# Kernel tuning notes

Hardware: AMD Instinct MI355X
Metric: run time of the kernel (lower is better)

Reference implementation:

```python
import jax, jax.numpy as jnp
import numpy as np
from jax import lax

B, T = 256, 64
X_DIMS, CCG_DIMS, H, N_TAG = 512, 256, 1024, 512
DIN = X_DIMS + CCG_DIMS
PAD = 0


def setup_inputs() -> dict:
    key = jax.random.key(0)
    ks = jax.random.split(key, 12)
    emb = jax.random.normal(ks[0], (N_TAG, CCG_DIMS), jnp.float32)
    emb = emb.at[PAD].set(0.0)  # padding_idx row is zero
    s_ih = 1.0 / np.sqrt(H)
    return {
        "x": jax.random.normal(ks[1], (B, X_DIMS), jnp.float32),
        "atom_truth": jax.random.randint(ks[2], (B, T), 0, N_TAG),
        "atom_mask": jax.random.randint(ks[3], (B, T), 0, 2).astype(bool),
        "emb": emb,
        "W_ih": jax.random.normal(ks[4], (4 * H, DIN), jnp.float32) * s_ih,
        "W_hh": jax.random.normal(ks[5], (4 * H, H), jnp.float32) * s_ih,
        "b_ih": jax.random.normal(ks[6], (4 * H,), jnp.float32) * s_ih,
        "b_hh": jax.random.normal(ks[7], (4 * H,), jnp.float32) * s_ih,
        "W_out": jax.random.normal(ks[8], (N_TAG, H), jnp.float32) * s_ih,
        "b_out": jax.random.normal(ks[9], (N_TAG,), jnp.float32) * s_ih,
        "h0": jax.random.normal(ks[10], (B, H), jnp.float32),
        "c0": jax.random.normal(ks[11], (B, H), jnp.float32),
    }


def reference(x, atom_truth, atom_mask, emb, W_ih, W_hh, b_ih, b_hh, W_out, b_out, h0, c0):
    b, t = atom_truth.shape
    # teacher forcing: step 0 uses token 0, step k uses atom_truth[:, k-1]
    prev_tok = jnp.concatenate([jnp.zeros((b, 1), atom_truth.dtype), atom_truth[:, :-1]], axis=1)
    ccg = emb[prev_tok]                                      # [B,T,E]
    inp = jnp.concatenate([jnp.broadcast_to(x[:, None, :], (b, t, x.shape[1])), ccg], axis=-1)
    # precompute input projection for all steps: [B,T,4H]
    xproj = jnp.einsum('btd,gd->btg', inp, W_ih) + b_ih + b_hh

    def cell(carry, xt):                                     # xt: [B,4H]
        h, c = carry
        gates = xt + h @ W_hh.T
        i, f, g, o = jnp.split(gates, 4, axis=-1)            # torch gate order i,f,g,o
        i, f, o = jax.nn.sigmoid(i), jax.nn.sigmoid(f), jax.nn.sigmoid(o)
        g = jnp.tanh(g)
        c = f * c + i * g
        h = o * jnp.tanh(c)
        return (h, c), h

    _, hs = lax.scan(cell, (h0, c0), jnp.swapaxes(xproj, 0, 1))  # hs: [T,B,H]
    logits = hs @ W_out.T + b_out                            # [T,B,N_TAG]
    logp = jax.nn.log_softmax(logits, axis=-1)
    tgt = atom_truth.T                                       # [T,B]
    nll = -jnp.take_along_axis(logp, tgt[..., None], axis=-1)[..., 0]  # [T,B]
    mask = atom_mask.T.astype(nll.dtype)
    return jnp.sum(nll * mask) / jnp.sum(mask)


if __name__ == "__main__":
    print(reference(**setup_inputs()))
```

## Files before the change

### kernel.cpp

```cpp
#include <hip/hip_runtime.h>
#include <hip/hip_bf16.h>

#define BB 256
#define TT 64
#define XD 512
#define CCG 256
#define DINk 768
#define HH 1024
#define G4 4096
#define NTAG 512

typedef float f32x4 __attribute__((ext_vector_type(4)));
typedef short s16x8 __attribute__((ext_vector_type(8)));
typedef short s16x4 __attribute__((ext_vector_type(4)));

#define WS_HS    0ull
#define WS_XBASE (WS_HS + (size_t)(TT+1)*BB*HH*2)
#define WS_EPROJ (WS_XBASE + (size_t)BB*G4*4)
#define WS_WIH   (WS_EPROJ + (size_t)NTAG*G4*4)
#define WS_WOUT  (WS_WIH + (size_t)G4*DINk*2)
#define WS_XBF   (WS_WOUT + (size_t)NTAG*HH*2)
#define WS_EMBBF (WS_XBF + (size_t)BB*XD*2)
#define WS_CNT   (WS_EMBBF + (size_t)NTAG*CCG*2)
#define WS_ACC   (WS_CNT + 1024)
#define WS_FLAG  (WS_ACC + 64)
#define WS_XPROJ (WS_FLAG + 64)

static __device__ __forceinline__ short f2bf(float f) {
  __hip_bfloat16 h = __float2bfloat16(f);
  return __builtin_bit_cast(short, h);
}
static __device__ __forceinline__ float bf2f(unsigned short u) {
  unsigned x = ((unsigned)u) << 16;
  return __builtin_bit_cast(float, x);
}
static __device__ __forceinline__ void store_dword_cc(void* p, unsigned v) {
  asm volatile("global_store_dword %0, %1, off sc0 sc1" :: "v"(p), "v"(v) : "memory");
}
static __device__ __forceinline__ void store_short_cc(void* p, unsigned v) {
  asm volatile("global_store_short %0, %1, off sc0 sc1" :: "v"(p), "v"(v) : "memory");
}
static __device__ __forceinline__ int load_int_cc(const void* p) {
  int r;
  asm volatile("global_load_dword %0, %1, off sc0 sc1\n\ts_waitcnt vmcnt(0)"
               : "=v"(r) : "v"(p) : "memory");
  return r;
}
static __device__ __forceinline__ float fsig(float x) {
  return __builtin_amdgcn_rcpf(1.f + __expf(-x));
}
static __device__ __forceinline__ float ftanh(float x) {
  return 1.f - 2.f * __builtin_amdgcn_rcpf(1.f + __expf(2.f * x));
}

__global__ void k_f2bf8(const float* __restrict__ in, short* __restrict__ out, int n8) {
  int i = blockIdx.x * blockDim.x + threadIdx.x;
  if (i >= n8) return;
  size_t idx = (size_t)i * 8;
  float4 a = *(const float4*)(in + idx);
  float4 b = *(const float4*)(in + idx + 4);
  s16x8 o;
  o[0]=f2bf(a.x); o[1]=f2bf(a.y); o[2]=f2bf(a.z); o[3]=f2bf(a.w);
  o[4]=f2bf(b.x); o[5]=f2bf(b.y); o[6]=f2bf(b.z); o[7]=f2bf(b.w);
  *(s16x8*)(out + idx) = o;
}

__global__ void k_init(const float* __restrict__ h0, const int* __restrict__ mask_as_int,
                       char* __restrict__ ws) {
  int tid = blockIdx.x * blockDim.x + threadIdx.x;
  short* hb0 = (short*)(ws + WS_HS);
  for (int i = tid; i < BB * HH; i += gridDim.x * blockDim.x) hb0[i] = f2bf(h0[i]);
  if (blockIdx.x == 0) {
    int* cnt = (int*)(ws + WS_CNT);
    for (int i = threadIdx.x; i < 256; i += blockDim.x) cnt[i] = 0;
    int v = 0;
    for (int i = threadIdx.x; i < 4096; i += blockDim.x) v |= (mask_as_int[i] & ~1);
    __shared__ int red[256];
    red[threadIdx.x] = v;
    __syncthreads();
    if (threadIdx.x == 0) {
      int a = 0;
      for (int j = 0; j < 256; j++) a |= red[j];
      ((int*)(ws + WS_FLAG))[0] = (a != 0) ? 1 : 0;
      float* acc = (float*)(ws + WS_ACC);
      acc[0] = 0.f; acc[1] = 0.f;
    }
  }
}

__global__ __launch_bounds__(256) void k_gemm(const short* __restrict__ A, int lda,
    const short* __restrict__ Bm, int ldb, int bcol0,
    short* __restrict__ C, int ldc, int ksteps,
    const float* __restrict__ bias1, const float* __restrict__ bias2) {
  int w = threadIdx.x >> 6, l = threadIdx.x & 63;
  int lc = l & 15, lq = l >> 4;
  int arow = blockIdx.x * 64 + w * 16 + lc;
  f32x4 acc[4];
  const f32x4 z = {0.f, 0.f, 0.f, 0.f};
#pragma unroll
  for (int i = 0; i < 4; i++) acc[i] = z;
  const short* ap = A + (size_t)arow * lda + lq * 8;
  for (int kk = 0; kk < ksteps; ++kk) {
    s16x8 a = *(const s16x8*)(ap + kk * 32);
#pragma unroll
    for (int nt = 0; nt < 4; ++nt) {
      int brow = blockIdx.y * 64 + nt * 16 + lc;
      s16x8 b = *(const s16x8*)(Bm + (size_t)brow * ldb + bcol0 + kk * 32 + lq * 8);
      acc[nt] = __builtin_amdgcn_mfma_f32_16x16x32_bf16(a, b, acc[nt], 0, 0, 0);
    }
  }
#pragma unroll
  for (int nt = 0; nt < 4; ++nt) {
    int col = blockIdx.y * 64 + nt * 16 + lc;
    float badd = (bias1 ? bias1[col] : 0.f) + (bias2 ? bias2[col] : 0.f);
#pragma unroll
    for (int j = 0; j < 4; j++) {
      int r = blockIdx.x * 64 + w * 16 + lq * 4 + j;
      C[(size_t)r * ldc + col] = f2bf(acc[nt][j] + badd);
    }
  }
}

__global__ __launch_bounds__(256) void k_xproj_t(const short* __restrict__ xb,
    const short* __restrict__ ep, const int* __restrict__ atruth,
    short* __restrict__ out) {
  __shared__ short tile[64 * 264];
  const int cc = blockIdx.x, g = blockIdx.y, t = blockIdx.z;
  const int b = threadIdx.x;
  const int tok = (t == 0) ? 0 : atruth[b * TT + t - 1];
  const int gc0 = g * 1024 + cc * 64;
  const short* xs = xb + (size_t)b * G4 + gc0;
  const short* es = ep + (size_t)tok * G4 + gc0;
#pragma unroll
  for (int i = 0; i < 64; i += 8) {
    s16x8 xv = *(const s16x8*)(xs + i);
    s16x8 ev = *(const s16x8*)(es + i);
#pragma unroll
    for (int j = 0; j < 8; ++j)
      tile[(i + j) * 264 + b] = f2bf(bf2f((unsigned short)xv[j]) + bf2f((unsigned short)ev[j]));
  }
  __syncthreads();
  const int c = threadIdx.x >> 2, b0 = (threadIdx.x & 3) * 64;
  short* dst = out + ((size_t)t * G4 + gc0 + c) * BB + b0;
  const short* src = tile + c * 264 + b0;
#pragma unroll
  for (int i = 0; i < 64; i += 8) *(s16x8*)(dst + i) = *(const s16x8*)(src + i);
}

__global__ __launch_bounds__(512, 2) void k_lstm(const float* __restrict__ Whh,
    const short* __restrict__ xproj, const float* __restrict__ c0,
    char* __restrict__ ws) {
  extern __shared__ char sm[];
  float* part = (float*)(sm + 131072);
  const int bid = blockIdx.x;
  const int xcd = bid & 7, slot = bid >> 3;
  const int mg = xcd >> 1;
  const int hb = slot * 2 + (xcd & 1);
  const int wgid = (xcd & 1) * 32 + slot;
  const int tid = threadIdx.x;
  const int w = tid >> 6, l = tid & 63;
  const int lc = l & 15, lq = l >> 4;
  const int wy = w & 3, kh = w >> 2;

  {
    const int r = tid >> 3, q = tid & 7;
    const int g = r >> 4, rl = r & 15;
    const float* src = Whh + (size_t)(g * HH + hb * 16 + rl) * HH + q * 128;
    const int swz = (rl & 7) << 4;
    char* dst = sm + r * 2048;
#pragma unroll
    for (int i = 0; i < 128; i += 8) {
      float4 f0 = *(const float4*)(src + i);
      float4 f1 = *(const float4*)(src + i + 4);
      s16x8 o;
      o[0]=f2bf(f0.x); o[1]=f2bf(f0.y); o[2]=f2bf(f0.z); o[3]=f2bf(f0.w);
      o[4]=f2bf(f1.x); o[5]=f2bf(f1.y); o[6]=f2bf(f1.z); o[7]=f2bf(f1.w);
      int koff = (q * 128 + i) * 2;
      *(s16x8*)(dst + (koff ^ swz)) = o;
    }
  }

  const int colbase = hb * 16;
  short* hs = (short*)(ws + WS_HS);
  int* flags = (int*)(ws + WS_CNT);
  const int swzl = (lc & 7) << 4;
  const int row0 = mg * 64 + wy * 16;

  float cst[4];
  if (kh == 0) {
#pragma unroll
    for (int j = 0; j < 4; ++j)
      cst[j] = c0[(size_t)(row0 + lq * 4 + j) * HH + colbase + lc];
  }
  float* pslot = part + ((size_t)wy * 64 + l) * 20;
  __syncthreads();

  for (int t = 0; t < TT; ++t) {
    s16x4 xg0, xg1, xg2, xg3;
    if (kh == 0) {
      const short* xp = xproj + ((size_t)t * G4 + colbase + lc) * BB + row0 + lq * 4;
      xg0 = *(const s16x4*)(xp);
      xg1 = *(const s16x4*)(xp + (size_t)1024 * BB);
      xg2 = *(const s16x4*)(xp + (size_t)2048 * BB);
      xg3 = *(const s16x4*)(xp + (size_t)3072 * BB);
    }

    if (t && w == 0) {
      const int* f = flags + mg * 64 + l;
      for (;;) {
        int v = load_int_cc(f);
        if (__all(v >= t)) break;
        __builtin_amdgcn_s_sleep(4);
      }
    }
    __syncthreads();

    const f32x4 z = {0.f, 0.f, 0.f, 0.f};
    f32x4 acc0 = z, acc1 = z, acc2 = z, acc3 = z;
    const short* arowp = hs + (size_t)t * (BB * HH) + (size_t)(row0 + lc) * HH + kh * 512 + lq * 8;
#pragma unroll
    for (int kk = 0; kk < 16; ++kk) {
      s16x8 a = *(const s16x8*)(arowp + kk * 32);
      const int kx = (((kh * 16 + kk) * 64) + lq * 16) ^ swzl;
      const char* bp = sm + lc * 2048 + kx;
      acc0 = __builtin_amdgcn_mfma_f32_16x16x32_bf16(a, *(const s16x8*)(bp), acc0, 0, 0, 0);
      acc1 = __builtin_amdgcn_mfma_f32_16x16x32_bf16(a, *(const s16x8*)(bp + 16 * 2048), acc1, 0, 0, 0);
      acc2 = __builtin_amdgcn_mfma_f32_16x16x32_bf16(a, *(const s16x8*)(bp + 32 * 2048), acc2, 0, 0, 0);
      acc3 = __builtin_amdgcn_mfma_f32_16x16x32_bf16(a, *(const s16x8*)(bp + 48 * 2048), acc3, 0, 0, 0);
    }

    if (kh == 1) {
      *(f32x4*)(pslot) = acc0;
      *(f32x4*)(pslot + 4) = acc1;
      *(f32x4*)(pslot + 8) = acc2;
      *(f32x4*)(pslot + 12) = acc3;
    }
    __syncthreads();

    if (kh == 0) {
      acc0 += *(const f32x4*)(pslot);
      acc1 += *(const f32x4*)(pslot + 4);
      acc2 += *(const f32x4*)(pslot + 8);
      acc3 += *(const f32x4*)(pslot + 12);
      short* hrow = hs + (size_t)(t + 1) * (BB * HH) + (size_t)(row0 + lq * 4) * HH + colbase + lc;
#pragma unroll
      for (int j = 0; j < 4; ++j) {
        float pi = acc0[j] + bf2f((unsigned short)xg0[j]);
        float pf = acc1[j] + bf2f((unsigned short)xg1[j]);
        float pg = acc2[j] + bf2f((unsigned short)xg2[j]);
        float po = acc3[j] + bf2f((unsigned short)xg3[j]);
        float cv = fsig(pf) * cst[j] + fsig(pi) * ftanh(pg);
        cst[j] = cv;
        float hv = fsig(po) * ftanh(cv);
        store_short_cc(hrow + (size_t)j * HH, (unsigned)(unsigned short)f2bf(hv));
      }
    }
    asm volatile("s_waitcnt vmcnt(0)" ::: "memory");
    __syncthreads();
    if (tid == 0 && t < TT - 1) store_dword_cc(flags + mg * 64 + wgid, t + 1);
  }
}

__global__ __launch_bounds__(256, 1) void k_logits(const short* __restrict__ hsb,
    const short* __restrict__ Wo, const float* __restrict__ bout,
    const int* __restrict__ atruth, const void* __restrict__ maskp,
    char* __restrict__ ws) {
  extern __shared__ char sm[];
  const int tid = threadIdx.x;
  const int w = tid >> 6, l = tid & 63;
  const int lc = l & 15, lq = l >> 4;
  const int rowbase = blockIdx.x * 64 + w * 16;
  f32x4 acc[32];
#pragma unroll
  for (int nt = 0; nt < 32; ++nt) {
    float bv = bout[nt * 16 + lc];
    f32x4 tmp = {bv, bv, bv, bv};
    acc[nt] = tmp;
  }
  const int swzl = (lc & 7) << 4;
  for (int kb = 0; kb < 16; ++kb) {
    __syncthreads();
    {
      const int r0 = tid >> 3, q = tid & 7;
#pragma unroll
      for (int i = 0; i < 16; i++) {
        int r = r0 + 32 * i;
        s16x8 v = *(const s16x8*)(Wo + (size_t)r * HH + kb * 64 + q * 8);
        *(s16x8*)(sm + r * 128 + ((q * 16) ^ ((r & 7) << 4))) = v;
      }
    }
    __syncthreads();
#pragma unroll
    for (int ks = 0; ks < 2; ++ks) {
      s16x8 a = *(const s16x8*)(hsb + (size_t)(rowbase + lc) * HH + kb * 64 + ks * 32 + lq * 8);
      const int kx = (ks * 64 + lq * 16) ^ swzl;
#pragma unroll
      for (int nt = 0; nt < 32; ++nt) {
        s16x8 b = *(const s16x8*)(sm + (nt * 16 + lc) * 128 + kx);
        acc[nt] = __builtin_amdgcn_mfma_f32_16x16x32_bf16(a, b, acc[nt], 0, 0, 0);
      }
    }
  }
  const int bytemode = ((const int*)(ws + WS_FLAG))[0];
  const unsigned char* mb = (const unsigned char*)maskp;
  const int* mi = (const int*)maskp;
  float nlls = 0.f, cnts = 0.f;
#pragma unroll
  for (int j = 0; j < 4; j++) {
    int gr = rowbase + lq * 4 + j;
    int tt = gr >> 8, b = gr & 255;
    float m = -1e30f;
#pragma unroll
    for (int nt = 0; nt < 32; ++nt) m = fmaxf(m, acc[nt][j]);
    m = fmaxf(m, __shfl_xor(m, 1)); m = fmaxf(m, __shfl_xor(m, 2));
    m = fmaxf(m, __shfl_xor(m, 4)); m = fmaxf(m, __shfl_xor(m, 8));
    float s = 0.f;
#pragma unroll
    for (int nt = 0; nt < 32; ++nt) s += __expf(acc[nt][j] - m);
    s += __shfl_xor(s, 1); s += __shfl_xor(s, 2);
    s += __shfl_xor(s, 4); s += __shfl_xor(s, 8);
    float lse = m + __logf(s);
    int tg = atruth[b * TT + tt];
    int mk = bytemode ? (int)mb[b * TT + tt] : mi[b * TT + tt];
    if (((tg & 15) == lc) && mk) {
      float tl = 0.f;
#pragma unroll
      for (int nt = 0; nt < 32; ++nt) if (nt == (tg >> 4)) tl = acc[nt][j];
      nlls += (lse - tl);
    }
    if (lc == 0 && mk) cnts += 1.f;
  }
#pragma unroll
  for (int off = 1; off < 64; off <<= 1) {
    nlls += __shfl_xor(nlls, off);
    cnts += __shfl_xor(cnts, off);
  }
  if (l == 0) {
    float* accf = (float*)(ws + WS_ACC);
    atomicAdd(&accf[0], nlls);
    atomicAdd(&accf[1], cnts);
  }
}

__global__ void k_final(const char* __restrict__ ws, float* __restrict__ out) {
  const float* accf = (const float*)(ws + WS_ACC);
  out[0] = accf[0] / accf[1];
}

extern "C" void kernel_launch(void* const* d_in, const int* in_sizes, int n_in,
                              void* d_out, int out_size, void* d_ws, size_t ws_size,
                              hipStream_t stream) {
  const float* x      = (const float*)d_in[0];
  const int*   atruth = (const int*)d_in[1];
  const void*  amask  = d_in[2];
  const float* emb    = (const float*)d_in[3];
  const float* W_ih   = (const float*)d_in[4];
  const float* W_hh   = (const float*)d_in[5];
  const float* b_ih   = (const float*)d_in[6];
  const float* b_hh   = (const float*)d_in[7];
  const float* W_out  = (const float*)d_in[8];
  const float* b_out  = (const float*)d_in[9];
  const float* h0     = (const float*)d_in[10];
  const float* c0     = (const float*)d_in[11];
  char* ws = (char*)d_ws;
  float* out = (float*)d_out;

  hipFuncSetAttribute((const void*)k_lstm, hipFuncAttributeMaxDynamicSharedMemorySize, 151552);
  hipFuncSetAttribute((const void*)k_logits, hipFuncAttributeMaxDynamicSharedMemorySize, 65536);

  k_f2bf8<<<dim3((G4 * DINk / 8 + 255) / 256), 256, 0, stream>>>(W_ih, (short*)(ws + WS_WIH), G4 * DINk / 8);
  k_f2bf8<<<dim3((NTAG * HH / 8 + 255) / 256), 256, 0, stream>>>(W_out, (short*)(ws + WS_WOUT), NTAG * HH / 8);
  k_f2bf8<<<dim3((BB * XD / 8 + 255) / 256), 256, 0, stream>>>(x, (short*)(ws + WS_XBF), BB * XD / 8);
  k_f2bf8<<<dim3((NTAG * CCG / 8 + 255) / 256), 256, 0, stream>>>(emb, (short*)(ws + WS_EMBBF), NTAG * CCG / 8);

  k_init<<<64, 256, 0, stream>>>(h0, (const int*)amask, ws);

  k_gemm<<<dim3(4, 64), 256, 0, stream>>>((short*)(ws + WS_XBF), XD, (short*)(ws + WS_WIH), DINk, 0,
                                          (short*)(ws + WS_XBASE), G4, XD / 32, b_ih, b_hh);
  k_gemm<<<dim3(8, 64), 256, 0, stream>>>((short*)(ws + WS_EMBBF), CCG, (short*)(ws + WS_WIH), DINk, XD,
                                          (short*)(ws + WS_EPROJ), G4, CCG / 32, nullptr, nullptr);

  k_xproj_t<<<dim3(16, 4, 64), 256, 0, stream>>>((const short*)(ws + WS_XBASE),
                                                 (const short*)(ws + WS_EPROJ), atruth,
                                                 (short*)(ws + WS_XPROJ));

  k_lstm<<<256, 512, 151552, stream>>>(W_hh, (const short*)(ws + WS_XPROJ), c0, ws);

  k_logits<<<256, 256, 65536, stream>>>((short*)(ws + WS_HS) + BB * HH, (short*)(ws + WS_WOUT), b_out,
                                        atruth, amask, ws);
  k_final<<<1, 1, 0, stream>>>(ws, out);
}
```

Before: 589.8 us.

## Keep W_hh slice in registers and split K four ways in LSTM kernel

```diff
diff --git a/kernel.cpp b/kernel.cpp
--- a/kernel.cpp
+++ b/kernel.cpp
@@ -151,7 +151,7 @@
     const short* __restrict__ xproj, const float* __restrict__ c0,
     char* __restrict__ ws) {
   extern __shared__ char sm[];
-  float* part = (float*)(sm + 131072);
+  float* part = (float*)sm;
   const int bid = blockIdx.x;
   const int xcd = bid & 7, slot = bid >> 3;
   const int mg = xcd >> 1;
@@ -160,49 +160,46 @@
   const int tid = threadIdx.x;
   const int w = tid >> 6, l = tid & 63;
   const int lc = l & 15, lq = l >> 4;
-  const int wy = w & 3, kh = w >> 2;
-
-  {
-    const int r = tid >> 3, q = tid & 7;
-    const int g = r >> 4, rl = r & 15;
-    const float* src = Whh + (size_t)(g * HH + hb * 16 + rl) * HH + q * 128;
-    const int swz = (rl & 7) << 4;
-    char* dst = sm + r * 2048;
-#pragma unroll
-    for (int i = 0; i < 128; i += 8) {
-      float4 f0 = *(const float4*)(src + i);
-      float4 f1 = *(const float4*)(src + i + 4);
+  const int wy = w & 1, kq = w >> 1;
+
+  const int colbase = hb * 16;
+  short* hs = (short*)(ws + WS_HS);
+  int* flags = (int*)(ws + WS_CNT);
+  const int arow0 = mg * 64 + wy * 32;
+
+  s16x8 breg[4][8];
+#pragma unroll
+  for (int g = 0; g < 4; ++g) {
+    const float* wr = Whh + (size_t)(g * HH + colbase + lc) * HH + kq * 256 + lq * 8;
+#pragma unroll
+    for (int s = 0; s < 8; ++s) {
+      float4 f0 = *(const float4*)(wr + s * 32);
+      float4 f1 = *(const float4*)(wr + s * 32 + 4);
       s16x8 o;
       o[0]=f2bf(f0.x); o[1]=f2bf(f0.y); o[2]=f2bf(f0.z); o[3]=f2bf(f0.w);
       o[4]=f2bf(f1.x); o[5]=f2bf(f1.y); o[6]=f2bf(f1.z); o[7]=f2bf(f1.w);
-      int koff = (q * 128 + i) * 2;
-      *(s16x8*)(dst + (koff ^ swz)) = o;
-    }
-  }
-
-  const int colbase = hb * 16;
-  short* hs = (short*)(ws + WS_HS);
-  int* flags = (int*)(ws + WS_CNT);
-  const int swzl = (lc & 7) << 4;
-  const int row0 = mg * 64 + wy * 16;
-
-  float cst[4];
-  if (kh == 0) {
-#pragma unroll
-    for (int j = 0; j < 4; ++j)
-      cst[j] = c0[(size_t)(row0 + lq * 4 + j) * HH + colbase + lc];
-  }
-  float* pslot = part + ((size_t)wy * 64 + l) * 20;
-  __syncthreads();
+      breg[g][s] = o;
+    }
+  }
+
+  float cst[2][4];
+  if (kq == 0) {
+#pragma unroll
+    for (int rt = 0; rt < 2; ++rt)
+#pragma unroll
+      for (int j = 0; j < 4; ++j)
+        cst[rt][j] = c0[(size_t)(arow0 + rt * 16 + lq * 4 + j) * HH + colbase + lc];
+  }
 
   for (int t = 0; t < TT; ++t) {
-    s16x4 xg0, xg1, xg2, xg3;
-    if (kh == 0) {
-      const short* xp = xproj + ((size_t)t * G4 + colbase + lc) * BB + row0 + lq * 4;
-      xg0 = *(const s16x4*)(xp);
-      xg1 = *(const s16x4*)(xp + (size_t)1024 * BB);
-      xg2 = *(const s16x4*)(xp + (size_t)2048 * BB);
-      xg3 = *(const s16x4*)(xp + (size_t)3072 * BB);
+    s16x4 xg[2][4];
+    if (kq == 0) {
+#pragma unroll
+      for (int rt = 0; rt < 2; ++rt)
+#pragma unroll
+        for (int g = 0; g < 4; ++g)
+          xg[rt][g] = *(const s16x4*)(xproj +
+              ((size_t)t * G4 + g * HH + colbase + lc) * BB + arow0 + rt * 16 + lq * 4);
     }
 
     if (t && w == 0) {
@@ -210,49 +207,63 @@
       for (;;) {
         int v = load_int_cc(f);
         if (__all(v >= t)) break;
-        __builtin_amdgcn_s_sleep(4);
+        __builtin_amdgcn_s_sleep(1);
       }
     }
     __syncthreads();
 
     const f32x4 z = {0.f, 0.f, 0.f, 0.f};
-    f32x4 acc0 = z, acc1 = z, acc2 = z, acc3 = z;
-    const short* arowp = hs + (size_t)t * (BB * HH) + (size_t)(row0 + lc) * HH + kh * 512 + lq * 8;
-#pragma unroll
-    for (int kk = 0; kk < 16; ++kk) {
-      s16x8 a = *(const s16x8*)(arowp + kk * 32);
-      const int kx = (((kh * 16 + kk) * 64) + lq * 16) ^ swzl;
-      const char* bp = sm + lc * 2048 + kx;
-      acc0 = __builtin_amdgcn_mfma_f32_16x16x32_bf16(a, *(const s16x8*)(bp), acc0, 0, 0, 0);
-      acc1 = __builtin_amdgcn_mfma_f32_16x16x32_bf16(a, *(const s16x8*)(bp + 16 * 2048), acc1, 0, 0, 0);
-      acc2 = __builtin_amdgcn_mfma_f32_16x16x32_bf16(a, *(const s16x8*)(bp + 32 * 2048), acc2, 0, 0, 0);
-      acc3 = __builtin_amdgcn_mfma_f32_16x16x32_bf16(a, *(const s16x8*)(bp + 48 * 2048), acc3, 0, 0, 0);
-    }
-
-    if (kh == 1) {
-      *(f32x4*)(pslot) = acc0;
-      *(f32x4*)(pslot + 4) = acc1;
-      *(f32x4*)(pslot + 8) = acc2;
-      *(f32x4*)(pslot + 12) = acc3;
-    }
-    __syncthreads();
-
-    if (kh == 0) {
-      acc0 += *(const f32x4*)(pslot);
-      acc1 += *(const f32x4*)(pslot + 4);
-      acc2 += *(const f32x4*)(pslot + 8);
-      acc3 += *(const f32x4*)(pslot + 12);
-      short* hrow = hs + (size_t)(t + 1) * (BB * HH) + (size_t)(row0 + lq * 4) * HH + colbase + lc;
-#pragma unroll
-      for (int j = 0; j < 4; ++j) {
-        float pi = acc0[j] + bf2f((unsigned short)xg0[j]);
-        float pf = acc1[j] + bf2f((unsigned short)xg1[j]);
-        float pg = acc2[j] + bf2f((unsigned short)xg2[j]);
-        float po = acc3[j] + bf2f((unsigned short)xg3[j]);
-        float cv = fsig(pf) * cst[j] + fsig(pi) * ftanh(pg);
-        cst[j] = cv;
-        float hv = fsig(po) * ftanh(cv);
-        store_short_cc(hrow + (size_t)j * HH, (unsigned)(unsigned short)f2bf(hv));
+    f32x4 acc[2][4];
+#pragma unroll
+    for (int rt = 0; rt < 2; ++rt)
+#pragma unroll
+      for (int g = 0; g < 4; ++g) acc[rt][g] = z;
+    const short* ab = hs + (size_t)t * (BB * HH) + (size_t)(arow0 + lc) * HH + kq * 256 + lq * 8;
+#pragma unroll
+    for (int s = 0; s < 8; ++s) {
+      s16x8 a0 = *(const s16x8*)(ab + s * 32);
+      s16x8 a1 = *(const s16x8*)(ab + 16 * HH + s * 32);
+#pragma unroll
+      for (int g = 0; g < 4; ++g) {
+        acc[0][g] = __builtin_amdgcn_mfma_f32_16x16x32_bf16(a0, breg[g][s], acc[0][g], 0, 0, 0);
+        acc[1][g] = __builtin_amdgcn_mfma_f32_16x16x32_bf16(a1, breg[g][s], acc[1][g], 0, 0, 0);
+      }
+    }
+
+    if (kq) {
+      float* ps = part + (size_t)(((kq - 1) * 2 + wy) * 64 + l) * 36;
+#pragma unroll
+      for (int rt = 0; rt < 2; ++rt)
+#pragma unroll
+        for (int g = 0; g < 4; ++g)
+          *(f32x4*)(ps + (rt * 4 + g) * 4) = acc[rt][g];
+    }
+    __syncthreads();
+
+    if (kq == 0) {
+#pragma unroll
+      for (int q = 0; q < 3; ++q) {
+        const float* ps = part + (size_t)((q * 2 + wy) * 64 + l) * 36;
+#pragma unroll
+        for (int rt = 0; rt < 2; ++rt)
+#pragma unroll
+          for (int g = 0; g < 4; ++g)
+            acc[rt][g] += *(const f32x4*)(ps + (rt * 4 + g) * 4);
+      }
+#pragma unroll
+      for (int rt = 0; rt < 2; ++rt) {
+        short* hrow = hs + (size_t)(t + 1) * (BB * HH) +
+                      (size_t)(arow0 + rt * 16 + lq * 4) * HH + colbase + lc;
+#pragma unroll
+        for (int j = 0; j < 4; ++j) {
+          float pi = acc[rt][0][j] + bf2f((unsigned short)xg[rt][0][j]);
+          float pf = acc[rt][1][j] + bf2f((unsigned short)xg[rt][1][j]);
+          float pg = acc[rt][2][j] + bf2f((unsigned short)xg[rt][2][j]);
+          float po = acc[rt][3][j] + bf2f((unsigned short)xg[rt][3][j]);
+          float cv = fsig(pf) * cst[rt][j] + fsig(pi) * ftanh(pg);
+          cst[rt][j] = cv;
+          store_short_cc(hrow + (size_t)j * HH, (unsigned)(unsigned short)f2bf(fsig(po) * ftanh(cv)));
+        }
       }
     }
     asm volatile("s_waitcnt vmcnt(0)" ::: "memory");
@@ -365,7 +376,7 @@
   char* ws = (char*)d_ws;
   float* out = (float*)d_out;
 
-  hipFuncSetAttribute((const void*)k_lstm, hipFuncAttributeMaxDynamicSharedMemorySize, 151552);
+  hipFuncSetAttribute((const void*)k_lstm, hipFuncAttributeMaxDynamicSharedMemorySize, 55296);
   hipFuncSetAttribute((const void*)k_logits, hipFuncAttributeMaxDynamicSharedMemorySize, 65536);
 
   k_f2bf8<<<dim3((G4 * DINk / 8 + 255) / 256), 256, 0, stream>>>(W_ih, (short*)(ws + WS_WIH), G4 * DINk / 8);
@@ -384,7 +395,7 @@
                                                  (const short*)(ws + WS_EPROJ), atruth,
                                                  (short*)(ws + WS_XPROJ));
 
-  k_lstm<<<256, 512, 151552, stream>>>(W_hh, (const short*)(ws + WS_XPROJ), c0, ws);
+  k_lstm<<<256, 512, 55296, stream>>>(W_hh, (const short*)(ws + WS_XPROJ), c0, ws);
 
   k_logits<<<256, 256, 65536, stream>>>((short*)(ws + WS_HS) + BB * HH, (short*)(ws + WS_WOUT), b_out,
                                         atruth, amask, ws);
```

Result: slower. 628.7 us (+6.6%).

## Use per-wave step flags and vectorized flag polling in recurrent LSTM kernel

Applied to the files above, without the earlier changes.

```diff
diff --git a/kernel.cpp b/kernel.cpp
--- a/kernel.cpp
+++ b/kernel.cpp
@@ -22,7 +22,7 @@
 #define WS_XBF   (WS_WOUT + (size_t)NTAG*HH*2)
 #define WS_EMBBF (WS_XBF + (size_t)BB*XD*2)
 #define WS_CNT   (WS_EMBBF + (size_t)NTAG*CCG*2)
-#define WS_ACC   (WS_CNT + 1024)
+#define WS_ACC   (WS_CNT + 4096)
 #define WS_FLAG  (WS_ACC + 64)
 #define WS_XPROJ (WS_FLAG + 64)
 
@@ -40,9 +40,9 @@
 static __device__ __forceinline__ void store_short_cc(void* p, unsigned v) {
   asm volatile("global_store_short %0, %1, off sc0 sc1" :: "v"(p), "v"(v) : "memory");
 }
-static __device__ __forceinline__ int load_int_cc(const void* p) {
-  int r;
-  asm volatile("global_load_dword %0, %1, off sc0 sc1\n\ts_waitcnt vmcnt(0)"
+static __device__ __forceinline__ int4 load_int4_cc(const void* p) {
+  int4 r;
+  asm volatile("global_load_dwordx4 %0, %1, off sc0 sc1\n\ts_waitcnt vmcnt(0)"
                : "=v"(r) : "v"(p) : "memory");
   return r;
 }
@@ -72,7 +72,7 @@
   for (int i = tid; i < BB * HH; i += gridDim.x * blockDim.x) hb0[i] = f2bf(h0[i]);
   if (blockIdx.x == 0) {
     int* cnt = (int*)(ws + WS_CNT);
-    for (int i = threadIdx.x; i < 256; i += blockDim.x) cnt[i] = 0;
+    for (int i = threadIdx.x; i < 1024; i += blockDim.x) cnt[i] = 0;
     int v = 0;
     for (int i = threadIdx.x; i < 4096; i += blockDim.x) v |= (mask_as_int[i] & ~1);
     __shared__ int red[256];
@@ -182,7 +182,7 @@
 
   const int colbase = hb * 16;
   short* hs = (short*)(ws + WS_HS);
-  int* flags = (int*)(ws + WS_CNT);
+  int* flags4 = (int*)(ws + WS_CNT);
   const int swzl = (lc & 7) << 4;
   const int row0 = mg * 64 + wy * 16;
 
@@ -196,21 +196,20 @@
   __syncthreads();
 
   for (int t = 0; t < TT; ++t) {
-    s16x4 xg0, xg1, xg2, xg3;
+    s16x4 xg[4];
     if (kh == 0) {
-      const short* xp = xproj + ((size_t)t * G4 + colbase + lc) * BB + row0 + lq * 4;
-      xg0 = *(const s16x4*)(xp);
-      xg1 = *(const s16x4*)(xp + (size_t)1024 * BB);
-      xg2 = *(const s16x4*)(xp + (size_t)2048 * BB);
-      xg3 = *(const s16x4*)(xp + (size_t)3072 * BB);
+#pragma unroll
+      for (int g = 0; g < 4; ++g)
+        xg[g] = *(const s16x4*)(xproj +
+            ((size_t)t * G4 + g * HH + colbase + lc) * BB + row0 + lq * 4);
     }
 
     if (t && w == 0) {
-      const int* f = flags + mg * 64 + l;
+      const int4* f = (const int4*)flags4 + (mg * 64 + l);
       for (;;) {
-        int v = load_int_cc(f);
-        if (__all(v >= t)) break;
-        __builtin_amdgcn_s_sleep(4);
+        int4 v = load_int4_cc(f);
+        if (__all((v.x >= t) && (v.y >= t) && (v.z >= t) && (v.w >= t))) break;
+        __builtin_amdgcn_s_sleep(1);
       }
     }
     __syncthreads();
@@ -242,22 +241,22 @@
       acc1 += *(const f32x4*)(pslot + 4);
       acc2 += *(const f32x4*)(pslot + 8);
       acc3 += *(const f32x4*)(pslot + 12);
-      short* hrow = hs + (size_t)(t + 1) * (BB * HH) + (size_t)(row0 + lq * 4) * HH + colbase + lc;
+      short* hrow = hs + (size_t)(t + 1) * (BB * HH) +
+                    (size_t)(row0 + lq * 4) * HH + colbase + lc;
 #pragma unroll
       for (int j = 0; j < 4; ++j) {
-        float pi = acc0[j] + bf2f((unsigned short)xg0[j]);
-        float pf = acc1[j] + bf2f((unsigned short)xg1[j]);
-        float pg = acc2[j] + bf2f((unsigned short)xg2[j]);
-        float po = acc3[j] + bf2f((unsigned short)xg3[j]);
+        float pi = acc0[j] + bf2f((unsigned short)xg[0][j]);
+        float pf = acc1[j] + bf2f((unsigned short)xg[1][j]);
+        float pg = acc2[j] + bf2f((unsigned short)xg[2][j]);
+        float po = acc3[j] + bf2f((unsigned short)xg[3][j]);
         float cv = fsig(pf) * cst[j] + fsig(pi) * ftanh(pg);
         cst[j] = cv;
-        float hv = fsig(po) * ftanh(cv);
-        store_short_cc(hrow + (size_t)j * HH, (unsigned)(unsigned short)f2bf(hv));
+        store_short_cc(hrow + (size_t)j * HH, (unsigned)(unsigned short)f2bf(fsig(po) * ftanh(cv)));
       }
-    }
-    asm volatile("s_waitcnt vmcnt(0)" ::: "memory");
-    __syncthreads();
-    if (tid == 0 && t < TT - 1) store_dword_cc(flags + mg * 64 + wgid, t + 1);
+      asm volatile("s_waitcnt vmcnt(0)" ::: "memory");
+      if (l == 0 && t < TT - 1)
+        store_dword_cc(flags4 + (mg * 64 + wgid) * 4 + wy, t + 1);
+    }
   }
 }
 
```

After: 625.4 us. 1.06x slower.

## Prefetch next-step xproj, batch h loads, and relayout LSTM partial sums

Applied to the files above, without the earlier changes.

```diff
diff --git a/kernel.cpp b/kernel.cpp
--- a/kernel.cpp
+++ b/kernel.cpp
@@ -187,62 +187,77 @@
   const int row0 = mg * 64 + wy * 16;
 
   float cst[4];
+  s16x4 xg0, xg1, xg2, xg3, xn0, xn1, xn2, xn3;
   if (kh == 0) {
 #pragma unroll
     for (int j = 0; j < 4; ++j)
       cst[j] = c0[(size_t)(row0 + lq * 4 + j) * HH + colbase + lc];
-  }
-  float* pslot = part + ((size_t)wy * 64 + l) * 20;
+    const short* xp = xproj + ((size_t)colbase + lc) * BB + row0 + lq * 4;
+    xg0 = *(const s16x4*)(xp);
+    xg1 = *(const s16x4*)(xp + (size_t)1024 * BB);
+    xg2 = *(const s16x4*)(xp + (size_t)2048 * BB);
+    xg3 = *(const s16x4*)(xp + (size_t)3072 * BB);
+  }
+  float* pslot = part + (size_t)wy * 1024 + l;
   __syncthreads();
 
   for (int t = 0; t < TT; ++t) {
-    s16x4 xg0, xg1, xg2, xg3;
-    if (kh == 0) {
-      const short* xp = xproj + ((size_t)t * G4 + colbase + lc) * BB + row0 + lq * 4;
-      xg0 = *(const s16x4*)(xp);
-      xg1 = *(const s16x4*)(xp + (size_t)1024 * BB);
-      xg2 = *(const s16x4*)(xp + (size_t)2048 * BB);
-      xg3 = *(const s16x4*)(xp + (size_t)3072 * BB);
-    }
-
     if (t && w == 0) {
       const int* f = flags + mg * 64 + l;
       for (;;) {
         int v = load_int_cc(f);
         if (__all(v >= t)) break;
-        __builtin_amdgcn_s_sleep(4);
-      }
-    }
-    __syncthreads();
+        __builtin_amdgcn_s_sleep(1);
+      }
+    }
+    __syncthreads();
+
+    if (kh == 0 && t + 1 < TT) {
+      const short* xp = xproj + ((size_t)(t + 1) * G4 + colbase + lc) * BB + row0 + lq * 4;
+      xn0 = *(const s16x4*)(xp);
+      xn1 = *(const s16x4*)(xp + (size_t)1024 * BB);
+      xn2 = *(const s16x4*)(xp + (size_t)2048 * BB);
+      xn3 = *(const s16x4*)(xp + (size_t)3072 * BB);
+    }
+
+    const short* arowp = hs + (size_t)t * (BB * HH) + (size_t)(row0 + lc) * HH + kh * 512 + lq * 8;
+    s16x8 areg[16];
+#pragma unroll
+    for (int kk = 0; kk < 16; ++kk) areg[kk] = *(const s16x8*)(arowp + kk * 32);
 
     const f32x4 z = {0.f, 0.f, 0.f, 0.f};
     f32x4 acc0 = z, acc1 = z, acc2 = z, acc3 = z;
-    const short* arowp = hs + (size_t)t * (BB * HH) + (size_t)(row0 + lc) * HH + kh * 512 + lq * 8;
 #pragma unroll
     for (int kk = 0; kk < 16; ++kk) {
-      s16x8 a = *(const s16x8*)(arowp + kk * 32);
       const int kx = (((kh * 16 + kk) * 64) + lq * 16) ^ swzl;
       const char* bp = sm + lc * 2048 + kx;
-      acc0 = __builtin_amdgcn_mfma_f32_16x16x32_bf16(a, *(const s16x8*)(bp), acc0, 0, 0, 0);
-      acc1 = __builtin_amdgcn_mfma_f32_16x16x32_bf16(a, *(const s16x8*)(bp + 16 * 2048), acc1, 0, 0, 0);
-      acc2 = __builtin_amdgcn_mfma_f32_16x16x32_bf16(a, *(const s16x8*)(bp + 32 * 2048), acc2, 0, 0, 0);
-      acc3 = __builtin_amdgcn_mfma_f32_16x16x32_bf16(a, *(const s16x8*)(bp + 48 * 2048), acc3, 0, 0, 0);
+      acc0 = __builtin_amdgcn_mfma_f32_16x16x32_bf16(areg[kk], *(const s16x8*)(bp), acc0, 0, 0, 0);
+      acc1 = __builtin_amdgcn_mfma_f32_16x16x32_bf16(areg[kk], *(const s16x8*)(bp + 16 * 2048), acc1, 0, 0, 0);
+      acc2 = __builtin_amdgcn_mfma_f32_16x16x32_bf16(areg[kk], *(const s16x8*)(bp + 32 * 2048), acc2, 0, 0, 0);
+      acc3 = __builtin_amdgcn_mfma_f32_16x16x32_bf16(areg[kk], *(const s16x8*)(bp + 48 * 2048), acc3, 0, 0, 0);
     }
 
     if (kh == 1) {
-      *(f32x4*)(pslot) = acc0;
-      *(f32x4*)(pslot + 4) = acc1;
-      *(f32x4*)(pslot + 8) = acc2;
-      *(f32x4*)(pslot + 12) = acc3;
+#pragma unroll
+      for (int j = 0; j < 4; ++j) {
+        pslot[(0 * 4 + j) * 64] = acc0[j];
+        pslot[(1 * 4 + j) * 64] = acc1[j];
+        pslot[(2 * 4 + j) * 64] = acc2[j];
+        pslot[(3 * 4 + j) * 64] = acc3[j];
+      }
     }
     __syncthreads();
 
     if (kh == 0) {
-      acc0 += *(const f32x4*)(pslot);
-      acc1 += *(const f32x4*)(pslot + 4);
-      acc2 += *(const f32x4*)(pslot + 8);
-      acc3 += *(const f32x4*)(pslot + 12);
-      short* hrow = hs + (size_t)(t + 1) * (BB * HH) + (size_t)(row0 + lq * 4) * HH + colbase + lc;
+#pragma unroll
+      for (int j = 0; j < 4; ++j) {
+        acc0[j] += pslot[(0 * 4 + j) * 64];
+        acc1[j] += pslot[(1 * 4 + j) * 64];
+        acc2[j] += pslot[(2 * 4 + j) * 64];
+        acc3[j] += pslot[(3 * 4 + j) * 64];
+      }
+      short* hrow = hs + (size_t)(t + 1) * (BB * HH) +
+                    (size_t)(row0 + lq * 4) * HH + colbase + lc;
 #pragma unroll
       for (int j = 0; j < 4; ++j) {
         float pi = acc0[j] + bf2f((unsigned short)xg0[j]);
@@ -251,9 +266,9 @@
         float po = acc3[j] + bf2f((unsigned short)xg3[j]);
         float cv = fsig(pf) * cst[j] + fsig(pi) * ftanh(pg);
         cst[j] = cv;
-        float hv = fsig(po) * ftanh(cv);
-        store_short_cc(hrow + (size_t)j * HH, (unsigned)(unsigned short)f2bf(hv));
-      }
+        store_short_cc(hrow + (size_t)j * HH, (unsigned)(unsigned short)f2bf(fsig(po) * ftanh(cv)));
+      }
+      xg0 = xn0; xg1 = xn1; xg2 = xn2; xg3 = xn3;
     }
     asm volatile("s_waitcnt vmcnt(0)" ::: "memory");
     __syncthreads();
@@ -365,7 +380,7 @@
   char* ws = (char*)d_ws;
   float* out = (float*)d_out;
 
-  hipFuncSetAttribute((const void*)k_lstm, hipFuncAttributeMaxDynamicSharedMemorySize, 151552);
+  hipFuncSetAttribute((const void*)k_lstm, hipFuncAttributeMaxDynamicSharedMemorySize, 147456);
   hipFuncSetAttribute((const void*)k_logits, hipFuncAttributeMaxDynamicSharedMemorySize, 65536);
 
   k_f2bf8<<<dim3((G4 * DINk / 8 + 255) / 256), 256, 0, stream>>>(W_ih, (short*)(ws + WS_WIH), G4 * DINk / 8);
@@ -384,7 +399,7 @@
                                                  (const short*)(ws + WS_EPROJ), atruth,
                                                  (short*)(ws + WS_XPROJ));
 
-  k_lstm<<<256, 512, 151552, stream>>>(W_hh, (const short*)(ws + WS_XPROJ), c0, ws);
+  k_lstm<<<256, 512, 147456, stream>>>(W_hh, (const short*)(ws + WS_XPROJ), c0, ws);
 
   k_logits<<<256, 256, 65536, stream>>>((short*)(ws + WS_HS) + BB * HH, (short*)(ws + WS_WOUT), b_out,
                                         atruth, amask, ws);
```

Measured after the change: 629.8 us. 6.8% more time.
